# Optimization experiments

Hardware: AMD Instinct MI355X
Metric: run time of the kernel (lower is better)

Reference implementation:

```python
import jax, jax.numpy as jnp
import numpy as np

B, I, H = 32768, 512, 512


def _uniform(key, shape, fan_in):
    bound = 1.0 / np.sqrt(fan_in)
    return jax.random.uniform(key, shape, jnp.float32, -bound, bound)


def setup_inputs() -> dict:
    key = jax.random.key(0)
    ks = jax.random.split(key, 16)
    inp = {
        "x": jax.random.normal(ks[0], (B, I), jnp.float32),
        "h": jax.random.normal(ks[1], (B, H), jnp.float32),
        "c_prev": jax.random.normal(ks[2], (B, H), jnp.float32),
        # weights stored as [in, out] so we apply x @ W (transpose of torch layout)
        "Wxi": _uniform(ks[3], (I, H), I), "bxi": _uniform(ks[4], (H,), I),
        "Whi": _uniform(ks[5], (H, H), H),
        "Wxf": _uniform(ks[6], (I, H), I), "bxf": _uniform(ks[7], (H,), I),
        "Whf": _uniform(ks[8], (H, H), H),
        "Wxc": _uniform(ks[9], (I, H), I), "bxc": _uniform(ks[10], (H,), I),
        "Whc": _uniform(ks[11], (H, H), H),
        "Wxo": _uniform(ks[12], (I, H), I), "bxo": _uniform(ks[13], (H,), I),
        "Who": _uniform(ks[14], (H, H), H),
    }
    return inp


def reference(x, h, c_prev, Wxi, bxi, Whi, Wxf, bxf, Whf, Wxc, bxc, Whc, Wxo, bxo, Who):
    # Faithful to source: peephole (w_c) projections are dead code; the
    # forget path f*c_prev is computed then discarded, so c_next = i * tanh(.)
    i = jax.nn.sigmoid(x @ Wxi + bxi + h @ Whi)            # input gate
    f = jax.nn.sigmoid(x @ Wxf + bxf + h @ Whf)            # computed, unused (as in source)
    c_next = i * jnp.tanh(x @ Wxc + bxc + h @ Whc)         # NOTE: no f*c_prev term (source bug)
    o = jax.nn.sigmoid(x @ Wxo + bxo + h @ Who)            # output gate
    h_next = o * jnp.tanh(c_next)
    del f, c_prev  # unused, matching the original module's effective math
    return (h_next, c_next)
```

## Files before the change

### kernel.cpp

```cpp
#include <hip/hip_runtime.h>
#include <hip/hip_bf16.h>


typedef unsigned short u16;
typedef u16 u16x8 __attribute__((ext_vector_type(8)));
typedef __bf16 bf16x8 __attribute__((ext_vector_type(8)));
typedef float f32x4 __attribute__((ext_vector_type(4)));

#define B_DIM 32768
#define H_DIM 512
#define K_DIM 1024
#define BH_ELEMS (B_DIM * H_DIM)

__device__ __forceinline__ float bf2f(u16 u) {
    unsigned v = ((unsigned)u) << 16;
    float f;
    __builtin_memcpy(&f, &v, 4);
    return f;
}

__device__ __forceinline__ u16 f2bf16u(float f) {
    __hip_bfloat16 b = __float2bfloat16(f);
    u16 u;
    __builtin_memcpy(&u, &b, 2);
    return u;
}

__device__ __forceinline__ float fast_sigmoid(float x) {
    return 1.0f / (1.0f + __expf(-x));
}

__device__ __forceinline__ float fast_tanh(float x) {
    float e = __expf(-2.0f * fabsf(x));
    float r = (1.0f - e) / (1.0f + e);
    return x < 0.0f ? -r : r;
}

__global__ void probe_dtype(const unsigned* __restrict__ x, int* __restrict__ flag) {
    const int lane = threadIdx.x;
    const unsigned lo = x[lane] & 0xFFFFu;
    const unsigned e = (lo >> 7) & 0xFFu;
    const bool sane = (e >= 100u && e <= 140u) || (lo == 0u);
    const unsigned long long m = __ballot(sane);
    if (lane == 0) *flag = (__popcll(m) >= 48) ? 1 : 0;
}

__global__ void pack_weights(const void* __restrict__ Wxi, const void* __restrict__ Whi,
                             const void* __restrict__ Wxc, const void* __restrict__ Whc,
                             const void* __restrict__ Wxo, const void* __restrict__ Who,
                             const int* __restrict__ flag, u16* __restrict__ Wt)
{
    __shared__ u16 tile[32][33];
    const bool isbf = (*flag != 0);
    const int g = blockIdx.z >> 1, half = blockIdx.z & 1;
    const void* src;
    if (g == 0)      src = half ? Whi : Wxi;
    else if (g == 1) src = half ? Whc : Wxc;
    else             src = half ? Who : Wxo;
    const int kk = blockIdx.y * 32, nn = blockIdx.x * 32;
    const int tx = threadIdx.x, ty = threadIdx.y;
    if (isbf) {
        const u16* s = (const u16*)src;
#pragma unroll
        for (int i2 = 0; i2 < 4; ++i2)
            tile[ty + 8 * i2][tx] = s[(kk + ty + 8 * i2) * 512 + nn + tx];
    } else {
        const float* s = (const float*)src;
#pragma unroll
        for (int i2 = 0; i2 < 4; ++i2)
            tile[ty + 8 * i2][tx] = f2bf16u(s[(kk + ty + 8 * i2) * 512 + nn + tx]);
    }
    __syncthreads();
#pragma unroll
    for (int i2 = 0; i2 < 4; ++i2)
        Wt[(long)g * 524288 + (long)(nn + ty + 8 * i2) * 1024 + half * 512 + kk + tx]
            = tile[tx][ty + 8 * i2];
}

__global__ __launch_bounds__(256, 2) void lstm_gemm(
    const void* __restrict__ x, const void* __restrict__ h,
    const u16* __restrict__ Wt,
    const void* __restrict__ bxi, const void* __restrict__ bxc,
    const void* __restrict__ bxo, const int* __restrict__ flag,
    void* __restrict__ out)
{
    __shared__ __align__(16) u16 As[128 * 32];
    __shared__ __align__(16) u16 Bs[3 * 64 * 32];

    const bool isbf = (*flag != 0);
    const int tid    = threadIdx.x;
    const int lane   = tid & 63;
    const int wave   = tid >> 6;
    const int wave_m = wave & 1;
    const int wave_n = wave >> 1;
    const int m0 = blockIdx.y * 128;
    const int n0 = blockIdx.x * 64;

    const int trow = tid >> 2, tkc = (tid & 3) * 8;
    const long a_g0 = (long)(m0 + trow)      * 512 + tkc;
    const long a_g1 = (long)(m0 + 64 + trow) * 512 + tkc;
    const int  a_l0 = tid * 8;
    const int  a_l1 = 2048 + tid * 8;
    long b_g[3];
#pragma unroll
    for (int q = 0; q < 3; ++q)
        b_g[q] = (long)q * 524288 + (long)(n0 + trow) * 1024 + tkc;

    int a_ld[4];
#pragma unroll
    for (int mt = 0; mt < 4; ++mt)
        a_ld[mt] = (wave_m * 64 + mt * 16 + (lane & 15)) * 32 + (lane >> 4) * 8;
    int b_ld[3][2];
#pragma unroll
    for (int g = 0; g < 3; ++g)
#pragma unroll
        for (int nt = 0; nt < 2; ++nt)
            b_ld[g][nt] = g * 2048 + (wave_n * 32 + nt * 16 + (lane & 15)) * 32 + (lane >> 4) * 8;

    f32x4 acc[3][4][2];
    const f32x4 zero = {0.f, 0.f, 0.f, 0.f};
#pragma unroll
    for (int g = 0; g < 3; ++g)
#pragma unroll
        for (int mt = 0; mt < 4; ++mt)
#pragma unroll
            for (int nt = 0; nt < 2; ++nt)
                acc[g][mt][nt] = zero;

    for (int k0 = 0; k0 < K_DIM; k0 += 32) {
        const void* src = (k0 < 512) ? x : h;
        const long kadj = (k0 < 512) ? k0 : (k0 - 512);

        bf16x8 av0, av1, bv[3];
        if (isbf) {
            const u16* s = (const u16*)src + kadj;
            u16x8 t0 = *(const u16x8*)(s + a_g0);
            u16x8 t1 = *(const u16x8*)(s + a_g1);
            __builtin_memcpy(&av0, &t0, 16);
            __builtin_memcpy(&av1, &t1, 16);
        } else {
            const float* s = (const float*)src + kadj;
            f32x4 p0 = *(const f32x4*)(s + a_g0);
            f32x4 p1 = *(const f32x4*)(s + a_g0 + 4);
            f32x4 q0 = *(const f32x4*)(s + a_g1);
            f32x4 q1 = *(const f32x4*)(s + a_g1 + 4);
#pragma unroll
            for (int j = 0; j < 4; ++j) {
                av0[j] = (__bf16)p0[j]; av0[4 + j] = (__bf16)p1[j];
                av1[j] = (__bf16)q0[j]; av1[4 + j] = (__bf16)q1[j];
            }
        }
#pragma unroll
        for (int q = 0; q < 3; ++q) {
            u16x8 t = *(const u16x8*)(Wt + b_g[q] + k0);
            __builtin_memcpy(&bv[q], &t, 16);
        }

        __syncthreads();
        *(bf16x8*)&As[a_l0] = av0;
        *(bf16x8*)&As[a_l1] = av1;
#pragma unroll
        for (int q = 0; q < 3; ++q)
            *(bf16x8*)&Bs[q * 2048 + tid * 8] = bv[q];
        __syncthreads();

        bf16x8 af[4];
#pragma unroll
        for (int mt = 0; mt < 4; ++mt)
            af[mt] = *(const bf16x8*)&As[a_ld[mt]];
        bf16x8 bfr[3][2];
#pragma unroll
        for (int g = 0; g < 3; ++g)
#pragma unroll
            for (int nt = 0; nt < 2; ++nt)
                bfr[g][nt] = *(const bf16x8*)&Bs[b_ld[g][nt]];

#pragma unroll
        for (int g = 0; g < 3; ++g)
#pragma unroll
            for (int mt = 0; mt < 4; ++mt)
#pragma unroll
            for (int nt = 0; nt < 2; ++nt)
                acc[g][mt][nt] = __builtin_amdgcn_mfma_f32_16x16x32_bf16(
                    af[mt], bfr[g][nt], acc[g][mt][nt], 0, 0, 0);
    }

    const int colbase = n0 + wave_n * 32 + (lane & 15);
    float bi[2], bc[2], bo[2];
#pragma unroll
    for (int nt = 0; nt < 2; ++nt) {
        const int col = colbase + nt * 16;
        if (isbf) {
            bi[nt] = bf2f(((const u16*)bxi)[col]);
            bc[nt] = bf2f(((const u16*)bxc)[col]);
            bo[nt] = bf2f(((const u16*)bxo)[col]);
        } else {
            bi[nt] = ((const float*)bxi)[col];
            bc[nt] = ((const float*)bxc)[col];
            bo[nt] = ((const float*)bxo)[col];
        }
    }

    const int rowbase = m0 + wave_m * 64 + (lane >> 4) * 4;
#pragma unroll
    for (int mt = 0; mt < 4; ++mt)
#pragma unroll
        for (int nt = 0; nt < 2; ++nt)
#pragma unroll
            for (int r = 0; r < 4; ++r) {
                const int row = rowbase + mt * 16 + r;
                const int col = colbase + nt * 16;
                const float iv = fast_sigmoid(acc[0][mt][nt][r] + bi[nt]);
                const float cv = iv * fast_tanh(acc[1][mt][nt][r] + bc[nt]);
                const float ov = fast_sigmoid(acc[2][mt][nt][r] + bo[nt]);
                const float hv = ov * fast_tanh(cv);
                const long idx = (long)row * 512 + col;
                if (isbf) {
                    ((u16*)out)[idx]            = f2bf16u(hv);
                    ((u16*)out)[BH_ELEMS + idx] = f2bf16u(cv);
                } else {
                    ((float*)out)[idx]            = hv;
                    ((float*)out)[BH_ELEMS + idx] = cv;
                }
            }
}

extern "C" void kernel_launch(void* const* d_in, const int* in_sizes, int n_in,
                              void* d_out, int out_size, void* d_ws, size_t ws_size,
                              hipStream_t stream) {
    const void* x   = d_in[0];
    const void* h   = d_in[1];
    const void* Wxi = d_in[3];
    const void* bxi = d_in[4];
    const void* Whi = d_in[5];
    const void* Wxc = d_in[9];
    const void* bxc = d_in[10];
    const void* Whc = d_in[11];
    const void* Wxo = d_in[12];
    const void* bxo = d_in[13];
    const void* Who = d_in[14];

    int* flag = (int*)d_ws;
    u16* Wt   = (u16*)((char*)d_ws + 256);

    probe_dtype<<<1, 64, 0, stream>>>((const unsigned*)x, flag);
    pack_weights<<<dim3(16, 16, 6), dim3(32, 8), 0, stream>>>(
        Wxi, Whi, Wxc, Whc, Wxo, Who, flag, Wt);
    lstm_gemm<<<dim3(8, 256), dim3(256), 0, stream>>>(
        x, h, Wt, bxi, bxc, bxo, flag, d_out);
}
```

Measured before the change: 453.3 us.

## Pre-pack activations to bf16 and stream tiles via direct global-to-LDS loads

Adds a pre-pass that converts and concatenates x and h into one bf16 [B,1024] buffer in workspace. The GEMM then loads A and B tiles straight into LDS with global_load_lds, uses a 64-wide K step with an XOR-swizzled LDS layout, and remaps block indices to group tiles that share data. This targets the per-iteration register round-trip, the fp32-to-bf16 conversion inside the main loop, and LDS bank conflicts. It costs an extra pass over the activations plus workspace, and keeps the old kernel as a fallback when workspace is too small.

```diff
diff --git a/kernel.cpp b/kernel.cpp
--- a/kernel.cpp
+++ b/kernel.cpp
@@ -11,6 +11,12 @@
 #define H_DIM 512
 #define K_DIM 1024
 #define BH_ELEMS (B_DIM * H_DIM)
+#define U_ELEMS ((long)B_DIM * K_DIM)
+#define WT_BYTES (3u * 512u * 1024u * 2u)
+#define U_BYTES ((size_t)U_ELEMS * 2u)
+
+#define GLOBAL_AS(p) ((__attribute__((address_space(1))) void*)(p))
+#define LDS_AS(p)    ((__attribute__((address_space(3))) void*)(p))
 
 __device__ __forceinline__ float bf2f(u16 u) {
     unsigned v = ((unsigned)u) << 16;
@@ -34,6 +40,10 @@
     float e = __expf(-2.0f * fabsf(x));
     float r = (1.0f - e) / (1.0f + e);
     return x < 0.0f ? -r : r;
+}
+
+__device__ __forceinline__ void gload16(const u16* g, u16* l) {
+    __builtin_amdgcn_global_load_lds(GLOBAL_AS((u16*)g), LDS_AS(l), 16, 0, 0);
 }
 
 __global__ void probe_dtype(const unsigned* __restrict__ x, int* __restrict__ flag) {
@@ -77,15 +87,44 @@
             = tile[tx][ty + 8 * i2];
 }
 
-__global__ __launch_bounds__(256, 2) void lstm_gemm(
+__global__ __launch_bounds__(256) void pack_u(
     const void* __restrict__ x, const void* __restrict__ h,
-    const u16* __restrict__ Wt,
+    const int* __restrict__ flag, u16* __restrict__ U)
+{
+    const bool isbf = (*flag != 0);
+    const long stride = (long)gridDim.x * blockDim.x;
+    for (long t = (long)blockIdx.x * blockDim.x + threadIdx.x;
+         t < (U_ELEMS >> 3); t += stride) {
+        const long e = t << 3;
+        const int r = (int)(e >> 10);
+        const int k = (int)(e & 1023);
+        const void* src = (k < 512) ? x : h;
+        const long so = (long)r * 512 + (k & 511);
+        u16x8 o;
+        if (isbf) {
+            o = *(const u16x8*)((const u16*)src + so);
+        } else {
+            const float* s = (const float*)src + so;
+            f32x4 p0 = *(const f32x4*)s;
+            f32x4 p1 = *(const f32x4*)(s + 4);
+#pragma unroll
+            for (int j = 0; j < 4; ++j) {
+                o[j] = f2bf16u(p0[j]);
+                o[4 + j] = f2bf16u(p1[j]);
+            }
+        }
+        *(u16x8*)(U + e) = o;
+    }
+}
+
+__global__ __launch_bounds__(256, 2) void lstm_gemm_v2(
+    const u16* __restrict__ U, const u16* __restrict__ Wt,
     const void* __restrict__ bxi, const void* __restrict__ bxc,
     const void* __restrict__ bxo, const int* __restrict__ flag,
     void* __restrict__ out)
 {
-    __shared__ __align__(16) u16 As[128 * 32];
-    __shared__ __align__(16) u16 Bs[3 * 64 * 32];
+    __shared__ __align__(16) u16 As[128 * 64];
+    __shared__ __align__(16) u16 Bs[3 * 64 * 64];
 
     const bool isbf = (*flag != 0);
     const int tid    = threadIdx.x;
@@ -93,29 +132,44 @@
     const int wave   = tid >> 6;
     const int wave_m = wave & 1;
     const int wave_n = wave >> 1;
-    const int m0 = blockIdx.y * 128;
-    const int n0 = blockIdx.x * 64;
-
-    const int trow = tid >> 2, tkc = (tid & 3) * 8;
-    const long a_g0 = (long)(m0 + trow)      * 512 + tkc;
-    const long a_g1 = (long)(m0 + 64 + trow) * 512 + tkc;
-    const int  a_l0 = tid * 8;
-    const int  a_l1 = 2048 + tid * 8;
-    long b_g[3];
-#pragma unroll
-    for (int q = 0; q < 3; ++q)
-        b_g[q] = (long)q * 524288 + (long)(n0 + trow) * 1024 + tkc;
-
-    int a_ld[4];
-#pragma unroll
-    for (int mt = 0; mt < 4; ++mt)
-        a_ld[mt] = (wave_m * 64 + mt * 16 + (lane & 15)) * 32 + (lane >> 4) * 8;
-    int b_ld[3][2];
+
+    const int swz = (blockIdx.x & 7) * 256 + (blockIdx.x >> 3);
+    const int m0 = (swz >> 3) * 128;
+    const int n0 = (swz & 7) * 64;
+
+    const int srow = lane >> 3;
+    const int sk2  = (lane & 7) ^ srow;
+    const u16* a_src[4];
+#pragma unroll
+    for (int j = 0; j < 4; ++j) {
+        const int ca = wave * 4 + j;
+        a_src[j] = U + (long)(m0 + ca * 8 + srow) * 1024 + sk2 * 8;
+    }
+    const u16* b_src[6];
+#pragma unroll
+    for (int q = 0; q < 6; ++q) {
+        const int cb = q * 4 + wave;
+        const int g = cb >> 3;
+        const int nrow = (cb & 7) * 8 + srow;
+        b_src[q] = Wt + (long)g * 524288 + (long)(n0 + nrow) * 1024 + sk2 * 8;
+    }
+
+    int a_off[4];
+#pragma unroll
+    for (int mt = 0; mt < 4; ++mt) {
+        const int row = wave_m * 64 + mt * 16 + (lane & 15);
+        const int p = (lane >> 4) ^ (row & 7);
+        a_off[mt] = row * 64 + p * 8;
+    }
+    int b_off[3][2];
 #pragma unroll
     for (int g = 0; g < 3; ++g)
 #pragma unroll
-        for (int nt = 0; nt < 2; ++nt)
-            b_ld[g][nt] = g * 2048 + (wave_n * 32 + nt * 16 + (lane & 15)) * 32 + (lane >> 4) * 8;
+        for (int nt = 0; nt < 2; ++nt) {
+            const int row = wave_n * 32 + nt * 16 + (lane & 15);
+            const int p = (lane >> 4) ^ (row & 7);
+            b_off[g][nt] = g * 4096 + row * 64 + p * 8;
+        }
 
     f32x4 acc[3][4][2];
     const f32x4 zero = {0.f, 0.f, 0.f, 0.f};
@@ -127,62 +181,38 @@
             for (int nt = 0; nt < 2; ++nt)
                 acc[g][mt][nt] = zero;
 
-    for (int k0 = 0; k0 < K_DIM; k0 += 32) {
-        const void* src = (k0 < 512) ? x : h;
-        const long kadj = (k0 < 512) ? k0 : (k0 - 512);
-
-        bf16x8 av0, av1, bv[3];
-        if (isbf) {
-            const u16* s = (const u16*)src + kadj;
-            u16x8 t0 = *(const u16x8*)(s + a_g0);
-            u16x8 t1 = *(const u16x8*)(s + a_g1);
-            __builtin_memcpy(&av0, &t0, 16);
-            __builtin_memcpy(&av1, &t1, 16);
-        } else {
-            const float* s = (const float*)src + kadj;
-            f32x4 p0 = *(const f32x4*)(s + a_g0);
-            f32x4 p1 = *(const f32x4*)(s + a_g0 + 4);
-            f32x4 q0 = *(const f32x4*)(s + a_g1);
-            f32x4 q1 = *(const f32x4*)(s + a_g1 + 4);
-#pragma unroll
-            for (int j = 0; j < 4; ++j) {
-                av0[j] = (__bf16)p0[j]; av0[4 + j] = (__bf16)p1[j];
-                av1[j] = (__bf16)q0[j]; av1[4 + j] = (__bf16)q1[j];
-            }
-        }
-#pragma unroll
-        for (int q = 0; q < 3; ++q) {
-            u16x8 t = *(const u16x8*)(Wt + b_g[q] + k0);
-            __builtin_memcpy(&bv[q], &t, 16);
-        }
-
+    for (int k0 = 0; k0 < K_DIM; k0 += 64) {
         __syncthreads();
-        *(bf16x8*)&As[a_l0] = av0;
-        *(bf16x8*)&As[a_l1] = av1;
-#pragma unroll
-        for (int q = 0; q < 3; ++q)
-            *(bf16x8*)&Bs[q * 2048 + tid * 8] = bv[q];
+#pragma unroll
+        for (int j = 0; j < 4; ++j)
+            gload16(a_src[j] + k0, &As[(wave * 4 + j) * 512]);
+#pragma unroll
+        for (int q = 0; q < 6; ++q)
+            gload16(b_src[q] + k0, &Bs[(q * 4 + wave) * 512]);
         __syncthreads();
 
-        bf16x8 af[4];
-#pragma unroll
-        for (int mt = 0; mt < 4; ++mt)
-            af[mt] = *(const bf16x8*)&As[a_ld[mt]];
-        bf16x8 bfr[3][2];
-#pragma unroll
-        for (int g = 0; g < 3; ++g)
-#pragma unroll
-            for (int nt = 0; nt < 2; ++nt)
-                bfr[g][nt] = *(const bf16x8*)&Bs[b_ld[g][nt]];
-
-#pragma unroll
-        for (int g = 0; g < 3; ++g)
+#pragma unroll
+        for (int kk = 0; kk < 2; ++kk) {
+            const int kx = kk * 32;
+            bf16x8 af[4];
 #pragma unroll
             for (int mt = 0; mt < 4; ++mt)
-#pragma unroll
-            for (int nt = 0; nt < 2; ++nt)
-                acc[g][mt][nt] = __builtin_amdgcn_mfma_f32_16x16x32_bf16(
-                    af[mt], bfr[g][nt], acc[g][mt][nt], 0, 0, 0);
+                af[mt] = *(const bf16x8*)&As[a_off[mt] ^ kx];
+            bf16x8 bfr[3][2];
+#pragma unroll
+            for (int g = 0; g < 3; ++g)
+#pragma unroll
+                for (int nt = 0; nt < 2; ++nt)
+                    bfr[g][nt] = *(const bf16x8*)&Bs[b_off[g][nt] ^ kx];
+#pragma unroll
+            for (int g = 0; g < 3; ++g)
+#pragma unroll
+                for (int mt = 0; mt < 4; ++mt)
+#pragma unroll
+                    for (int nt = 0; nt < 2; ++nt)
+                        acc[g][mt][nt] = __builtin_amdgcn_mfma_f32_16x16x32_bf16(
+                            af[mt], bfr[g][nt], acc[g][mt][nt], 0, 0, 0);
+        }
     }
 
     const int colbase = n0 + wave_n * 32 + (lane & 15);
@@ -225,6 +255,154 @@
             }
 }
 
+__global__ __launch_bounds__(256, 2) void lstm_gemm_fb(
+    const void* __restrict__ x, const void* __restrict__ h,
+    const u16* __restrict__ Wt,
+    const void* __restrict__ bxi, const void* __restrict__ bxc,
+    const void* __restrict__ bxo, const int* __restrict__ flag,
+    void* __restrict__ out)
+{
+    __shared__ __align__(16) u16 As[128 * 32];
+    __shared__ __align__(16) u16 Bs[3 * 64 * 32];
+
+    const bool isbf = (*flag != 0);
+    const int tid    = threadIdx.x;
+    const int lane   = tid & 63;
+    const int wave   = tid >> 6;
+    const int wave_m = wave & 1;
+    const int wave_n = wave >> 1;
+    const int m0 = blockIdx.y * 128;
+    const int n0 = blockIdx.x * 64;
+
+    const int trow = tid >> 2, tkc = (tid & 3) * 8;
+    const long a_g0 = (long)(m0 + trow)      * 512 + tkc;
+    const long a_g1 = (long)(m0 + 64 + trow) * 512 + tkc;
+    const int  a_l0 = tid * 8;
+    const int  a_l1 = 2048 + tid * 8;
+    long b_g[3];
+#pragma unroll
+    for (int q = 0; q < 3; ++q)
+        b_g[q] = (long)q * 524288 + (long)(n0 + trow) * 1024 + tkc;
+
+    int a_ld[4];
+#pragma unroll
+    for (int mt = 0; mt < 4; ++mt)
+        a_ld[mt] = (wave_m * 64 + mt * 16 + (lane & 15)) * 32 + (lane >> 4) * 8;
+    int b_ld[3][2];
+#pragma unroll
+    for (int g = 0; g < 3; ++g)
+#pragma unroll
+        for (int nt = 0; nt < 2; ++nt)
+            b_ld[g][nt] = g * 2048 + (wave_n * 32 + nt * 16 + (lane & 15)) * 32 + (lane >> 4) * 8;
+
+    f32x4 acc[3][4][2];
+    const f32x4 zero = {0.f, 0.f, 0.f, 0.f};
+#pragma unroll
+    for (int g = 0; g < 3; ++g)
+#pragma unroll
+        for (int mt = 0; mt < 4; ++mt)
+#pragma unroll
+            for (int nt = 0; nt < 2; ++nt)
+                acc[g][mt][nt] = zero;
+
+    for (int k0 = 0; k0 < K_DIM; k0 += 32) {
+        const void* src = (k0 < 512) ? x : h;
+        const long kadj = (k0 < 512) ? k0 : (k0 - 512);
+
+        bf16x8 av0, av1, bv[3];
+        if (isbf) {
+            const u16* s = (const u16*)src + kadj;
+            u16x8 t0 = *(const u16x8*)(s + a_g0);
+            u16x8 t1 = *(const u16x8*)(s + a_g1);
+            __builtin_memcpy(&av0, &t0, 16);
+            __builtin_memcpy(&av1, &t1, 16);
+        } else {
+            const float* s = (const float*)src + kadj;
+            f32x4 p0 = *(const f32x4*)(s + a_g0);
+            f32x4 p1 = *(const f32x4*)(s + a_g0 + 4);
+            f32x4 q0 = *(const f32x4*)(s + a_g1);
+            f32x4 q1 = *(const f32x4*)(s + a_g1 + 4);
+#pragma unroll
+            for (int j = 0; j < 4; ++j) {
+                av0[j] = (__bf16)p0[j]; av0[4 + j] = (__bf16)p1[j];
+                av1[j] = (__bf16)q0[j]; av1[4 + j] = (__bf16)q1[j];
+            }
+        }
+#pragma unroll
+        for (int q = 0; q < 3; ++q) {
+            u16x8 t = *(const u16x8*)(Wt + b_g[q] + k0);
+            __builtin_memcpy(&bv[q], &t, 16);
+        }
+
+        __syncthreads();
+        *(bf16x8*)&As[a_l0] = av0;
+        *(bf16x8*)&As[a_l1] = av1;
+#pragma unroll
+        for (int q = 0; q < 3; ++q)
+            *(bf16x8*)&Bs[q * 2048 + tid * 8] = bv[q];
+        __syncthreads();
+
+        bf16x8 af[4];
+#pragma unroll
+        for (int mt = 0; mt < 4; ++mt)
+            af[mt] = *(const bf16x8*)&As[a_ld[mt]];
+        bf16x8 bfr[3][2];
+#pragma unroll
+        for (int g = 0; g < 3; ++g)
+#pragma unroll
+            for (int nt = 0; nt < 2; ++nt)
+                bfr[g][nt] = *(const bf16x8*)&Bs[b_ld[g][nt]];
+
+#pragma unroll
+        for (int g = 0; g < 3; ++g)
+#pragma unroll
+            for (int mt = 0; mt < 4; ++mt)
+#pragma unroll
+            for (int nt = 0; nt < 2; ++nt)
+                acc[g][mt][nt] = __builtin_amdgcn_mfma_f32_16x16x32_bf16(
+                    af[mt], bfr[g][nt], acc[g][mt][nt], 0, 0, 0);
+    }
+
+    const int colbase = n0 + wave_n * 32 + (lane & 15);
+    float bi[2], bc[2], bo[2];
+#pragma unroll
+    for (int nt = 0; nt < 2; ++nt) {
+        const int col = colbase + nt * 16;
+        if (isbf) {
+            bi[nt] = bf2f(((const u16*)bxi)[col]);
+            bc[nt] = bf2f(((const u16*)bxc)[col]);
+            bo[nt] = bf2f(((const u16*)bxo)[col]);
+        } else {
+            bi[nt] = ((const float*)bxi)[col];
+            bc[nt] = ((const float*)bxc)[col];
+            bo[nt] = ((const float*)bxo)[col];
+        }
+    }
+
+    const int rowbase = m0 + wave_m * 64 + (lane >> 4) * 4;
+#pragma unroll
+    for (int mt = 0; mt < 4; ++mt)
+#pragma unroll
+        for (int nt = 0; nt < 2; ++nt)
+#pragma unroll
+            for (int r = 0; r < 4; ++r) {
+                const int row = rowbase + mt * 16 + r;
+                const int col = colbase + nt * 16;
+                const float iv = fast_sigmoid(acc[0][mt][nt][r] + bi[nt]);
+                const float cv = iv * fast_tanh(acc[1][mt][nt][r] + bc[nt]);
+                const float ov = fast_sigmoid(acc[2][mt][nt][r] + bo[nt]);
+                const float hv = ov * fast_tanh(cv);
+                const long idx = (long)row * 512 + col;
+                if (isbf) {
+                    ((u16*)out)[idx]            = f2bf16u(hv);
+                    ((u16*)out)[BH_ELEMS + idx] = f2bf16u(cv);
+                } else {
+                    ((float*)out)[idx]            = hv;
+                    ((float*)out)[BH_ELEMS + idx] = cv;
+                }
+            }
+}
+
 extern "C" void kernel_launch(void* const* d_in, const int* in_sizes, int n_in,
                               void* d_out, int out_size, void* d_ws, size_t ws_size,
                               hipStream_t stream) {
@@ -242,10 +420,19 @@
 
     int* flag = (int*)d_ws;
     u16* Wt   = (u16*)((char*)d_ws + 256);
+    const size_t need = 256 + (size_t)WT_BYTES + U_BYTES;
 
     probe_dtype<<<1, 64, 0, stream>>>((const unsigned*)x, flag);
     pack_weights<<<dim3(16, 16, 6), dim3(32, 8), 0, stream>>>(
         Wxi, Whi, Wxc, Whc, Wxo, Who, flag, Wt);
-    lstm_gemm<<<dim3(8, 256), dim3(256), 0, stream>>>(
-        x, h, Wt, bxi, bxc, bxo, flag, d_out);
-}
+
+    if (ws_size >= need) {
+        u16* U = (u16*)((char*)d_ws + 256 + WT_BYTES);
+        pack_u<<<dim3(4096), dim3(256), 0, stream>>>(x, h, flag, U);
+        lstm_gemm_v2<<<dim3(2048), dim3(256), 0, stream>>>(
+            U, Wt, bxi, bxc, bxo, flag, d_out);
+    } else {
+        lstm_gemm_fb<<<dim3(8, 256), dim3(256), 0, stream>>>(
+            x, h, Wt, bxi, bxc, bxo, flag, d_out);
+    }
+}
```

After: 390.7 us. 13.8% less time.
